# Kernel optimization log

Measured on AMD Instinct MI355X. Metric: run time of the kernel, lower is better.

The kernel has to match this reference:

```python
import jax, jax.numpy as jnp
import numpy as np

B, S, E, H = 64, 256, 1024, 16
D = E // H  # head dim = 64


def setup_inputs() -> dict:
    key = jax.random.key(0)
    ks = jax.random.split(key, 6)
    x = jax.random.normal(ks[0], (B, S, E), dtype=jnp.float32)
    # torch nn.MultiheadAttention packed in-projection [3E, E] and biases
    sc = 1.0 / np.sqrt(E)
    in_proj_w = jax.random.normal(ks[1], (3 * E, E), dtype=jnp.float32) * sc
    in_proj_b = jax.random.normal(ks[2], (3 * E,), dtype=jnp.float32) * 0.02
    out_proj_w = jax.random.normal(ks[3], (E, E), dtype=jnp.float32) * sc
    out_proj_b = jax.random.normal(ks[4], (E,), dtype=jnp.float32) * 0.02
    # spatial bias = exp(-dist^2 / (2*median)) in (0, 1], symmetric
    pos = jax.random.normal(ks[5], (S, 3), dtype=jnp.float32)
    dist = jnp.sqrt(jnp.sum((pos[:, None, :] - pos[None, :, :]) ** 2, -1) + 1e-12)
    med = jnp.median(dist)
    spatial_bias = jnp.exp(-dist ** 2 / (2.0 * med))
    return {"x": x, "in_proj_w": in_proj_w, "in_proj_b": in_proj_b,
            "out_proj_w": out_proj_w, "out_proj_b": out_proj_b,
            "spatial_bias": spatial_bias}


def reference(x, in_proj_w, in_proj_b, out_proj_w, out_proj_b, spatial_bias):
    # packed QKV projection: x [B,S,E] @ in_proj_w.T [E,3E]
    qkv = x @ in_proj_w.T + in_proj_b          # [B,S,3E]
    q, k, v = jnp.split(qkv, 3, axis=-1)       # each [B,S,E]
    q = q.reshape(B, S, H, D)
    k = k.reshape(B, S, H, D)
    v = v.reshape(B, S, H, D)
    scale = 1.0 / jnp.sqrt(jnp.asarray(D, dtype=x.dtype))
    # additive float attn_mask broadcast over batch & heads
    scores = jnp.einsum('bqhd,bkhd->bhqk', q, k) * scale + spatial_bias[None, None]
    attn = jax.nn.softmax(scores, axis=-1)     # [B,H,S,S]
    ctx = jnp.einsum('bhqk,bkhd->bqhd', attn, v).reshape(B, S, E)
    h = ctx @ out_proj_w.T + out_proj_b        # [B,S,E]
    return x + h
```

## Files before the change

kernel.cpp:

```cpp
#include <hip/hip_runtime.h>
#include <hip/hip_bf16.h>
#include <stdint.h>


typedef __attribute__((ext_vector_type(8))) __bf16 bf16x8;
typedef __attribute__((ext_vector_type(4))) float f32x4;

#define DEVI static __device__ __forceinline__

DEVI unsigned short f2bf(float f) {
  union { float f; unsigned u; } x; x.f = f;
  unsigned r = x.u + 0x7fffu + ((x.u >> 16) & 1u);
  return (unsigned short)(r >> 16);
}

typedef unsigned int __attribute__((address_space(1))) u32_g;
typedef unsigned int __attribute__((address_space(3))) u32_l;

DEVI void g2l16(const unsigned short* g, unsigned short* l) {
  __builtin_amdgcn_global_load_lds((const u32_g*)g, (u32_l*)l, 16, 0, 0);
}

__global__ __launch_bounds__(256) void cvt_kernel(const float* __restrict__ s,
                                                  unsigned short* __restrict__ d, int n) {
  int i = (blockIdx.x * 256 + threadIdx.x) * 4;
  if (i >= n) return;
  float4 v = *(const float4*)(s + i);
  ushort4 o;
  o.x = f2bf(v.x); o.y = f2bf(v.y); o.z = f2bf(v.z); o.w = f2bf(v.w);
  *(ushort4*)(d + i) = o;
}

template <int EPI>
__global__ __launch_bounds__(256, 2)
void gemm_bt(const unsigned short* __restrict__ A,
             const unsigned short* __restrict__ Bw,
             const float* __restrict__ bias,
             unsigned short* __restrict__ Qo,
             unsigned short* __restrict__ Ko,
             unsigned short* __restrict__ VTo,
             const float* __restrict__ Xres,
             float* __restrict__ Out) {
  __shared__ unsigned short As[8192];
  __shared__ unsigned short Bs[8192];
  const int lane = threadIdx.x & 63, wave = threadIdx.x >> 6;
  const int l15 = lane & 15, lg = lane >> 4;
  const int wr = wave >> 1, wc = wave & 1;
  const int am0 = blockIdx.x * 128, bn0 = blockIdx.y * 128;

  f32x4 acc[4][4] = {};

  for (int kt = 0; kt < 16; ++kt) {
    const int k0 = kt * 64;
#pragma unroll
    for (int i = 0; i < 4; ++i) {
      const int seg = wave * 4 + i;
      const int off = seg * 1024 + lane * 16;
      const int row = off >> 7;
      const int ke  = (off & 127) >> 1;
      g2l16(A  + (size_t)(am0 + row) * 1024 + k0 + ke, &As[seg * 512]);
      g2l16(Bw + (size_t)(bn0 + row) * 1024 + k0 + ke, &Bs[seg * 512]);
    }
    __syncthreads();
#pragma unroll
    for (int kk = 0; kk < 2; ++kk) {
      bf16x8 a[4], b[4];
#pragma unroll
      for (int mf = 0; mf < 4; ++mf)
        a[mf] = *(const bf16x8*)&As[(wr * 64 + mf * 16 + l15) * 64 + kk * 32 + lg * 8];
#pragma unroll
      for (int nf = 0; nf < 4; ++nf)
        b[nf] = *(const bf16x8*)&Bs[(wc * 64 + nf * 16 + l15) * 64 + kk * 32 + lg * 8];
#pragma unroll
      for (int mf = 0; mf < 4; ++mf)
#pragma unroll
        for (int nf = 0; nf < 4; ++nf)
          acc[mf][nf] = __builtin_amdgcn_mfma_f32_16x16x32_bf16(a[mf], b[nf], acc[mf][nf], 0, 0, 0);
    }
    __syncthreads();
  }

  if (EPI == 0) {
#pragma unroll
    for (int nf = 0; nf < 4; ++nf) {
      const int col = bn0 + wc * 64 + nf * 16 + l15;
      const int which = col >> 10;
      const int e = col & 1023;
      const int hh = e >> 6, dd = e & 63;
      const float bv = bias[col];
#pragma unroll
      for (int mf = 0; mf < 4; ++mf) {
        const int row0 = am0 + wr * 64 + mf * 16 + lg * 4;
        const int bb = row0 >> 8;
        const int s0 = row0 & 255;
        if (which == 2) {
          unsigned long long pk = 0;
#pragma unroll
          for (int r = 0; r < 4; ++r)
            pk |= (unsigned long long)f2bf(acc[mf][nf][r] + bv) << (16 * r);
          *(unsigned long long*)&VTo[((size_t)(bb * 16 + hh) * 64 + dd) * 256 + s0] = pk;
        } else {
          unsigned short* dst = (which == 0) ? Qo : Ko;
#pragma unroll
          for (int r = 0; r < 4; ++r)
            dst[((size_t)(bb * 16 + hh) * 256 + s0 + r) * 64 + dd] = f2bf(acc[mf][nf][r] + bv);
        }
      }
    }
  } else {
#pragma unroll
    for (int nf = 0; nf < 4; ++nf) {
      const int col = bn0 + wc * 64 + nf * 16 + l15;
      const float bv = bias[col];
#pragma unroll
      for (int mf = 0; mf < 4; ++mf) {
#pragma unroll
        for (int r = 0; r < 4; ++r) {
          const int row = am0 + wr * 64 + mf * 16 + lg * 4 + r;
          const size_t idx = (size_t)row * 1024 + col;
          Out[idx] = Xres[idx] + acc[mf][nf][r] + bv;
        }
      }
    }
  }
}

__global__ __launch_bounds__(256) void attn_kernel(const unsigned short* __restrict__ Qg,
                                                   const unsigned short* __restrict__ Kg,
                                                   const unsigned short* __restrict__ VTg,
                                                   const float* __restrict__ bias,
                                                   unsigned short* __restrict__ ctx) {
  __shared__ unsigned short P[4][64][80];
  const int lane = threadIdx.x & 63, wave = threadIdx.x >> 6;
  const int l15 = lane & 15, lg = lane >> 4;
  const int bh = blockIdx.x;
  const int bb = bh >> 4, hh = bh & 15;
  const size_t base = (size_t)bh * (256 * 64);
  const int q0 = wave * 64;

  bf16x8 qfr[4][2];
#pragma unroll
  for (int qi = 0; qi < 4; ++qi)
#pragma unroll
    for (int kc = 0; kc < 2; ++kc)
      qfr[qi][kc] = *(const bf16x8*)&Qg[base + (size_t)(q0 + qi * 16 + l15) * 64 + kc * 32 + lg * 8];

  f32x4 o[4][4] = {};
  float mrow[4], lrow[4];
#pragma unroll
  for (int i = 0; i < 4; ++i) { mrow[i] = -1e30f; lrow[i] = 0.f; }

  for (int c = 0; c < 4; ++c) {
    bf16x8 kfr[4][2];
#pragma unroll
    for (int kr = 0; kr < 4; ++kr)
#pragma unroll
      for (int kc = 0; kc < 2; ++kc)
        kfr[kr][kc] = *(const bf16x8*)&Kg[base + (size_t)(c * 64 + kr * 16 + l15) * 64 + kc * 32 + lg * 8];

    f32x4 s[4][4] = {};
#pragma unroll
    for (int kr = 0; kr < 4; ++kr)
#pragma unroll
      for (int qi = 0; qi < 4; ++qi)
#pragma unroll
        for (int kc = 0; kc < 2; ++kc)
          s[kr][qi] = __builtin_amdgcn_mfma_f32_16x16x32_bf16(kfr[kr][kc], qfr[qi][kc], s[kr][qi], 0, 0, 0);

    float cmax[4];
#pragma unroll
    for (int qi = 0; qi < 4; ++qi) cmax[qi] = -1e30f;
#pragma unroll
    for (int kr = 0; kr < 4; ++kr)
#pragma unroll
      for (int qi = 0; qi < 4; ++qi)
#pragma unroll
        for (int r = 0; r < 4; ++r) {
          const int krow = c * 64 + kr * 16 + lg * 4 + r;
          const int qcol = q0 + qi * 16 + l15;
          float v = s[kr][qi][r] * 0.125f + bias[qcol * 256 + krow];
          s[kr][qi][r] = v;
          cmax[qi] = fmaxf(cmax[qi], v);
        }
#pragma unroll
    for (int qi = 0; qi < 4; ++qi) {
      cmax[qi] = fmaxf(cmax[qi], __shfl_xor(cmax[qi], 16, 64));
      cmax[qi] = fmaxf(cmax[qi], __shfl_xor(cmax[qi], 32, 64));
    }
    float resc[4], csum[4];
#pragma unroll
    for (int qi = 0; qi < 4; ++qi) {
      float mn = fmaxf(mrow[qi], cmax[qi]);
      resc[qi] = __expf(mrow[qi] - mn);
      mrow[qi] = mn;
      csum[qi] = 0.f;
    }
#pragma unroll
    for (int kr = 0; kr < 4; ++kr)
#pragma unroll
      for (int qi = 0; qi < 4; ++qi)
#pragma unroll
        for (int r = 0; r < 4; ++r) {
          float e = __expf(s[kr][qi][r] - mrow[qi]);
          s[kr][qi][r] = e;
          csum[qi] += e;
        }
#pragma unroll
    for (int qi = 0; qi < 4; ++qi) {
      csum[qi] += __shfl_xor(csum[qi], 16, 64);
      csum[qi] += __shfl_xor(csum[qi], 32, 64);
      lrow[qi] = lrow[qi] * resc[qi] + csum[qi];
    }

#pragma unroll
    for (int kr = 0; kr < 4; ++kr)
#pragma unroll
      for (int qi = 0; qi < 4; ++qi)
#pragma unroll
        for (int r = 0; r < 4; ++r)
          P[wave][qi * 16 + l15][kr * 16 + lg * 4 + r] = f2bf(s[kr][qi][r]);
    asm volatile("s_waitcnt lgkmcnt(0)" ::: "memory");

#pragma unroll
    for (int qrf = 0; qrf < 4; ++qrf)
#pragma unroll
      for (int r = 0; r < 4; ++r) {
        float f = __shfl(resc[qrf], lg * 4 + r, 64);
#pragma unroll
        for (int df = 0; df < 4; ++df) o[qrf][df][r] *= f;
      }

    bf16x8 vb[2][4], pa[4][2];
#pragma unroll
    for (int kc = 0; kc < 2; ++kc)
#pragma unroll
      for (int df = 0; df < 4; ++df)
        vb[kc][df] = *(const bf16x8*)&VTg[base + (size_t)(df * 16 + l15) * 256 + c * 64 + kc * 32 + lg * 8];
#pragma unroll
    for (int qrf = 0; qrf < 4; ++qrf)
#pragma unroll
      for (int kc = 0; kc < 2; ++kc)
        pa[qrf][kc] = *(const bf16x8*)&P[wave][qrf * 16 + l15][kc * 32 + lg * 8];
#pragma unroll
    for (int qrf = 0; qrf < 4; ++qrf)
#pragma unroll
      for (int df = 0; df < 4; ++df)
#pragma unroll
        for (int kc = 0; kc < 2; ++kc)
          o[qrf][df] = __builtin_amdgcn_mfma_f32_16x16x32_bf16(pa[qrf][kc], vb[kc][df], o[qrf][df], 0, 0, 0);
  }

#pragma unroll
  for (int qrf = 0; qrf < 4; ++qrf)
#pragma unroll
    for (int r = 0; r < 4; ++r) {
      float li = __shfl(lrow[qrf], lg * 4 + r, 64);
      float inv = 1.0f / li;
      const int q = q0 + qrf * 16 + lg * 4 + r;
#pragma unroll
      for (int df = 0; df < 4; ++df) {
        const int d = df * 16 + l15;
        ctx[((size_t)(bb * 256 + q) * 16 + hh) * 64 + d] = f2bf(o[qrf][df][r] * inv);
      }
    }
}

extern "C" void kernel_launch(void* const* d_in, const int* in_sizes, int n_in,
                              void* d_out, int out_size, void* d_ws, size_t ws_size,
                              hipStream_t stream) {
  const float* x  = (const float*)d_in[0];
  const float* wi = (const float*)d_in[1];
  const float* bi = (const float*)d_in[2];
  const float* wo = (const float*)d_in[3];
  const float* bo = (const float*)d_in[4];
  const float* sb = (const float*)d_in[5];
  float* out = (float*)d_out;

  char* ws = (char*)d_ws;
  unsigned short* xbf  = (unsigned short*)(ws);
  unsigned short* winb = (unsigned short*)(ws + 33554432u);
  unsigned short* wob  = (unsigned short*)(ws + 39845888u);
  unsigned short* Qb   = (unsigned short*)(ws + 41943040u);
  unsigned short* Kb   = (unsigned short*)(ws + 75497472u);
  unsigned short* VTb  = (unsigned short*)(ws + 109051904u);
  unsigned short* ctx  = xbf;

  cvt_kernel<<<16384, 256, 0, stream>>>(x, xbf, 16777216);
  cvt_kernel<<<3072, 256, 0, stream>>>(wi, winb, 3145728);
  cvt_kernel<<<1024, 256, 0, stream>>>(wo, wob, 1048576);

  gemm_bt<0><<<dim3(128, 24), 256, 0, stream>>>(xbf, winb, bi, Qb, Kb, VTb, nullptr, nullptr);

  attn_kernel<<<1024, 256, 0, stream>>>(Qb, Kb, VTb, sb, ctx);

  gemm_bt<1><<<dim3(128, 8), 256, 0, stream>>>(ctx, wob, bo, nullptr, nullptr, nullptr, x, out);
}
```

Before: 308.3 us.

## Rewrite GEMMs as 256x256 multi-stage pipelined kernels with swizzled LDS

```diff
diff --git a/kernel.cpp b/kernel.cpp
--- a/kernel.cpp
+++ b/kernel.cpp
@@ -32,65 +32,101 @@
 }
 
 template <int EPI>
-__global__ __launch_bounds__(256, 2)
-void gemm_bt(const unsigned short* __restrict__ A,
-             const unsigned short* __restrict__ Bw,
-             const float* __restrict__ bias,
-             unsigned short* __restrict__ Qo,
-             unsigned short* __restrict__ Ko,
-             unsigned short* __restrict__ VTo,
-             const float* __restrict__ Xres,
-             float* __restrict__ Out) {
-  __shared__ unsigned short As[8192];
-  __shared__ unsigned short Bs[8192];
-  const int lane = threadIdx.x & 63, wave = threadIdx.x >> 6;
+__global__ __launch_bounds__(512, 2)
+void gemm8(const unsigned short* __restrict__ A,
+           const unsigned short* __restrict__ Bw,
+           const float* __restrict__ bias,
+           unsigned short* __restrict__ Qo,
+           unsigned short* __restrict__ Ko,
+           unsigned short* __restrict__ VTo,
+           const float* __restrict__ Xres,
+           float* __restrict__ Out) {
+  extern __shared__ unsigned short lds[];
+  const int lane = threadIdx.x & 63, wid = threadIdx.x >> 6;
   const int l15 = lane & 15, lg = lane >> 4;
-  const int wr = wave >> 1, wc = wave & 1;
-  const int am0 = blockIdx.x * 128, bn0 = blockIdx.y * 128;
-
-  f32x4 acc[4][4] = {};
-
-  for (int kt = 0; kt < 16; ++kt) {
-    const int k0 = kt * 64;
-#pragma unroll
-    for (int i = 0; i < 4; ++i) {
-      const int seg = wave * 4 + i;
-      const int off = seg * 1024 + lane * 16;
-      const int row = off >> 7;
-      const int ke  = (off & 127) >> 1;
-      g2l16(A  + (size_t)(am0 + row) * 1024 + k0 + ke, &As[seg * 512]);
-      g2l16(Bw + (size_t)(bn0 + row) * 1024 + k0 + ke, &Bs[seg * 512]);
-    }
-    __syncthreads();
-#pragma unroll
-    for (int kk = 0; kk < 2; ++kk) {
-      bf16x8 a[4], b[4];
-#pragma unroll
-      for (int mf = 0; mf < 4; ++mf)
-        a[mf] = *(const bf16x8*)&As[(wr * 64 + mf * 16 + l15) * 64 + kk * 32 + lg * 8];
-#pragma unroll
-      for (int nf = 0; nf < 4; ++nf)
-        b[nf] = *(const bf16x8*)&Bs[(wc * 64 + nf * 16 + l15) * 64 + kk * 32 + lg * 8];
-#pragma unroll
-      for (int mf = 0; mf < 4; ++mf)
-#pragma unroll
-        for (int nf = 0; nf < 4; ++nf)
-          acc[mf][nf] = __builtin_amdgcn_mfma_f32_16x16x32_bf16(a[mf], b[nf], acc[mf][nf], 0, 0, 0);
-    }
-    __syncthreads();
+  const int wr = wid >> 2, wcn = wid & 3;
+  const int am0 = blockIdx.x * 256, bn0 = blockIdx.y * 256;
+
+  const int srow0 = wid * 16 + (lane >> 2);
+  const int scb0  = (lane & 3) * 16;
+
+  f32x4 acc[8][4] = {};
+
+#define SWZ(row) ((((row) >> 1) & 3) << 4)
+
+#define STAGE(s) { \
+    const int slot_ = (s) & 3; \
+    _Pragma("unroll") \
+    for (int j = 0; j < 2; ++j) { \
+      const int row_ = j * 128 + srow0; \
+      const int cs_ = scb0 ^ SWZ(row_); \
+      g2l16(A  + (size_t)(am0 + row_) * 1024 + (s) * 32 + (cs_ >> 1), \
+            &lds[slot_ * 8192 + j * 4096 + wid * 512]); \
+      g2l16(Bw + (size_t)(bn0 + row_) * 1024 + (s) * 32 + (cs_ >> 1), \
+            &lds[32768 + slot_ * 8192 + j * 4096 + wid * 512]); \
+    } }
+
+#define LOADFRAGS(p) \
+    bf16x8 a[8], b[4]; \
+    { const unsigned short* As_ = &lds[((p) & 3) * 8192]; \
+      const unsigned short* Bs_ = &lds[32768 + ((p) & 3) * 8192]; \
+      _Pragma("unroll") \
+      for (int mf = 0; mf < 8; ++mf) { \
+        const int row_ = wr * 128 + mf * 16 + l15; \
+        a[mf] = *(const bf16x8*)((const char*)As_ + row_ * 64 + ((lg * 16) ^ SWZ(row_))); \
+      } \
+      _Pragma("unroll") \
+      for (int nf = 0; nf < 4; ++nf) { \
+        const int row_ = wcn * 64 + nf * 16 + l15; \
+        b[nf] = *(const bf16x8*)((const char*)Bs_ + row_ * 64 + ((lg * 16) ^ SWZ(row_))); \
+      } }
+
+#define MFMAS() { \
+    __builtin_amdgcn_s_setprio(1); \
+    _Pragma("unroll") \
+    for (int mf = 0; mf < 8; ++mf) \
+      _Pragma("unroll") \
+      for (int nf = 0; nf < 4; ++nf) \
+        acc[mf][nf] = __builtin_amdgcn_mfma_f32_16x16x32_bf16(a[mf], b[nf], acc[mf][nf], 0, 0, 0); \
+    __builtin_amdgcn_s_setprio(0); }
+
+  STAGE(0) STAGE(1) STAGE(2)
+  asm volatile("s_waitcnt vmcnt(8)" ::: "memory");
+  __builtin_amdgcn_s_barrier();
+
+#pragma unroll 4
+  for (int p = 0; p < 29; ++p) {
+    LOADFRAGS(p)
+    STAGE(p + 3)
+    asm volatile("s_waitcnt vmcnt(8)" ::: "memory");
+    asm volatile("s_waitcnt lgkmcnt(0)" ::: "memory");
+    __builtin_amdgcn_s_barrier();
+    MFMAS()
   }
+  { LOADFRAGS(29)
+    asm volatile("s_waitcnt vmcnt(4)" ::: "memory");
+    asm volatile("s_waitcnt lgkmcnt(0)" ::: "memory");
+    __builtin_amdgcn_s_barrier();
+    MFMAS() }
+  { LOADFRAGS(30)
+    asm volatile("s_waitcnt vmcnt(0)" ::: "memory");
+    asm volatile("s_waitcnt lgkmcnt(0)" ::: "memory");
+    __builtin_amdgcn_s_barrier();
+    MFMAS() }
+  { LOADFRAGS(31)
+    MFMAS() }
 
   if (EPI == 0) {
 #pragma unroll
     for (int nf = 0; nf < 4; ++nf) {
-      const int col = bn0 + wc * 64 + nf * 16 + l15;
+      const int col = bn0 + wcn * 64 + nf * 16 + l15;
       const int which = col >> 10;
       const int e = col & 1023;
       const int hh = e >> 6, dd = e & 63;
       const float bv = bias[col];
 #pragma unroll
-      for (int mf = 0; mf < 4; ++mf) {
-        const int row0 = am0 + wr * 64 + mf * 16 + lg * 4;
+      for (int mf = 0; mf < 8; ++mf) {
+        const int row0 = am0 + wr * 128 + mf * 16 + lg * 4;
         const int bb = row0 >> 8;
         const int s0 = row0 & 255;
         if (which == 2) {
@@ -110,19 +146,23 @@
   } else {
 #pragma unroll
     for (int nf = 0; nf < 4; ++nf) {
-      const int col = bn0 + wc * 64 + nf * 16 + l15;
+      const int col = bn0 + wcn * 64 + nf * 16 + l15;
       const float bv = bias[col];
 #pragma unroll
-      for (int mf = 0; mf < 4; ++mf) {
+      for (int mf = 0; mf < 8; ++mf) {
 #pragma unroll
         for (int r = 0; r < 4; ++r) {
-          const int row = am0 + wr * 64 + mf * 16 + lg * 4 + r;
+          const int row = am0 + wr * 128 + mf * 16 + lg * 4 + r;
           const size_t idx = (size_t)row * 1024 + col;
           Out[idx] = Xres[idx] + acc[mf][nf][r] + bv;
         }
       }
     }
   }
+#undef SWZ
+#undef STAGE
+#undef LOADFRAGS
+#undef MFMAS
 }
 
 __global__ __launch_bounds__(256) void attn_kernel(const unsigned short* __restrict__ Qg,
@@ -173,15 +213,17 @@
 #pragma unroll
     for (int kr = 0; kr < 4; ++kr)
 #pragma unroll
-      for (int qi = 0; qi < 4; ++qi)
+      for (int qi = 0; qi < 4; ++qi) {
+        const int krow0 = c * 64 + kr * 16 + lg * 4;
+        const int qcol = q0 + qi * 16 + l15;
+        const f32x4 b4 = *(const f32x4*)&bias[qcol * 256 + krow0];
 #pragma unroll
         for (int r = 0; r < 4; ++r) {
-          const int krow = c * 64 + kr * 16 + lg * 4 + r;
-          const int qcol = q0 + qi * 16 + l15;
-          float v = s[kr][qi][r] * 0.125f + bias[qcol * 256 + krow];
+          float v = s[kr][qi][r] * 0.125f + b4[r];
           s[kr][qi][r] = v;
           cmax[qi] = fmaxf(cmax[qi], v);
         }
+      }
 #pragma unroll
     for (int qi = 0; qi < 4; ++qi) {
       cmax[qi] = fmaxf(cmax[qi], __shfl_xor(cmax[qi], 16, 64));
@@ -285,13 +327,18 @@
   unsigned short* VTb  = (unsigned short*)(ws + 109051904u);
   unsigned short* ctx  = xbf;
 
+  (void)hipFuncSetAttribute(reinterpret_cast<const void*>(gemm8<0>),
+                            hipFuncAttributeMaxDynamicSharedMemorySize, 131072);
+  (void)hipFuncSetAttribute(reinterpret_cast<const void*>(gemm8<1>),
+                            hipFuncAttributeMaxDynamicSharedMemorySize, 131072);
+
   cvt_kernel<<<16384, 256, 0, stream>>>(x, xbf, 16777216);
   cvt_kernel<<<3072, 256, 0, stream>>>(wi, winb, 3145728);
   cvt_kernel<<<1024, 256, 0, stream>>>(wo, wob, 1048576);
 
-  gemm_bt<0><<<dim3(128, 24), 256, 0, stream>>>(xbf, winb, bi, Qb, Kb, VTb, nullptr, nullptr);
+  gemm8<0><<<dim3(64, 12), 512, 131072, stream>>>(xbf, winb, bi, Qb, Kb, VTb, nullptr, nullptr);
 
   attn_kernel<<<1024, 256, 0, stream>>>(Qb, Kb, VTb, sb, ctx);
 
-  gemm_bt<1><<<dim3(128, 8), 256, 0, stream>>>(ctx, wob, bo, nullptr, nullptr, nullptr, x, out);
-}
+  gemm8<1><<<dim3(64, 4), 512, 131072, stream>>>(ctx, wob, bo, nullptr, nullptr, nullptr, x, out);
+}
```

Result: faster. 292.8 us (-5.0%).
